# Optimization experiments

Measured on AMD Instinct MI355X. Metric: run time of the kernel, lower is better.

## Reference

```python
import jax, jax.numpy as jnp
import numpy as np

TAU = 10.0
AMP_FACTOR = 6.0
BLOCK = 10  # each pixel -> 8x8 value block padded by 1 -> 10x10


def _make_h(size=200, wavelength=5.32e-07, pixel_size=3.6e-05, distance=0.1):
    ll = pixel_size * size
    fi = 1.0 / ll
    wn = 2 * 3.1415926 / wavelength
    phi = np.fromfunction(
        lambda x, y: np.square((x - size // 2) * fi) + np.square((y - size // 2) * fi),
        shape=(size, size), dtype=np.float64)
    h = np.fft.fftshift(np.exp(1j * wn * distance) * np.exp(-1j * wavelength * np.pi * distance * phi))
    return h.astype(np.complex64)


def setup_inputs() -> dict:
    key = jax.random.key(0)
    B, S, P = 16, 200, 256
    ks = jax.random.split(key, 5)
    h = _make_h(size=S)
    return {
        "waves_real": jax.random.normal(ks[0], (B, S, S), jnp.float32),
        "waves_imag": jax.random.normal(ks[1], (B, S, S), jnp.float32),
        "h_real": jnp.asarray(h.real, jnp.float32),
        "h_imag": jnp.asarray(h.imag, jnp.float32),
        "voltage": jax.random.uniform(ks[2], (S, S, P), jnp.float32),
        "phase_func": jax.random.uniform(ks[3], (P,), jnp.float32),
        "intensity_func": jax.random.uniform(ks[4], (P,), jnp.float32),
    }


def _gumbel_softmax_hard(logits, key, tau):
    u = jax.random.uniform(key, logits.shape, logits.dtype, 1e-10, 1.0)
    g = -jnp.log(-jnp.log(u))
    y_soft = jax.nn.softmax((logits + g) / tau, axis=-1)
    y_hard = jax.nn.one_hot(jnp.argmax(y_soft, axis=-1), logits.shape[-1], dtype=logits.dtype)
    # straight-through estimator
    return y_hard + y_soft - jax.lax.stop_gradient(y_soft)


def reference(waves_real, waves_imag, h_real, h_imag, voltage, phase_func, intensity_func):
    waves = waves_real + 1j * waves_imag              # (B,S,S) complex
    h = h_real + 1j * h_imag                          # (S,S) complex transfer fn
    temp = jnp.fft.ifft2(jnp.fft.fft2(waves) * h)     # free-space diffraction

    k1, k2 = jax.random.split(jax.random.key(42))
    exp_j_phase = _gumbel_softmax_hard(voltage, k1, TAU) @ phase_func      # (S,S)
    amplitude = (_gumbel_softmax_hard(voltage, k2, TAU) @ intensity_func) * AMP_FACTOR
    phase_trig = amplitude * (jnp.cos(exp_j_phase) + 1j * jnp.sin(exp_j_phase))
    x = temp * phase_trig                             # (B,S,S) complex

    # pixel expansion: each pixel -> 10x10 block (value in center 8x8, zero border)
    B, S = x.shape[0], x.shape[1]
    pat = jnp.zeros((BLOCK, BLOCK), x.dtype).at[1:9, 1:9].set(1.0)
    out = (x[:, :, None, :, None] * pat[None, :, None, :][None]).reshape(B, S * BLOCK, S * BLOCK)
    return jnp.stack([out.real, out.imag], axis=-1)   # (B, 10S, 10S, 2) float
```

## Files before the change

kernel.cpp:

```cpp
#include <hip/hip_runtime.h>
#include <math.h>

constexpr int S = 200;
constexpr int SS = S * S;
constexpr int FLAT = 3200;
constexpr int SLICE = 640000;
constexpr int MP = 256;
constexpr int KP = 224;
constexpr int PS = MP * KP;

typedef short short8 __attribute__((ext_vector_type(8)));
typedef float float4v __attribute__((ext_vector_type(4)));

struct TFOut { unsigned a, b; };

__host__ __device__ constexpr TFOut tf2x32(unsigned k0, unsigned k1,
                                           unsigned x0, unsigned x1) {
  unsigned ks2 = k0 ^ k1 ^ 0x1BD11BDAu;
  unsigned ks[3] = {k0, k1, ks2};
  const int R0[4] = {13, 15, 26, 6};
  const int R1[4] = {17, 29, 16, 24};
  x0 += ks[0]; x1 += ks[1];
  for (int i = 0; i < 5; ++i) {
    const int* R = (i & 1) ? R1 : R0;
    for (int j = 0; j < 4; ++j) {
      x0 += x1;
      x1 = (x1 << R[j]) | (x1 >> (32 - R[j]));
      x1 ^= x0;
    }
    x0 += ks[(i + 1) % 3];
    x1 += ks[(i + 2) % 3] + (unsigned)(i + 1);
  }
  return {x0, x1};
}

constexpr TFOut KEY1 = tf2x32(0u, 42u, 0u, 0u);
constexpr TFOut KEY2 = tf2x32(0u, 42u, 0u, 1u);

__device__ inline float bits_to_u(unsigned bits) {
  float f = __uint_as_float((bits >> 9) | 0x3f800000u) - 1.0f;
  f = f + 1e-10f;
  return fmaxf(1e-10f, f);
}
__device__ inline float u_to_g_exact(float u) {
  float l1 = (float)log((double)u);
  float l2 = (float)log((double)(-l1));
  return -l2;
}
__device__ inline float u_to_g_fast(float u) {
  float l1 = logf(u);
  float l2 = logf(-l1);
  return -l2;
}
__device__ inline unsigned ordf(float f) {
  unsigned u = __float_as_uint(f);
  return (u & 0x80000000u) ? ~u : (u | 0x80000000u);
}
__device__ inline float unordf(unsigned u) {
  return (u & 0x80000000u) ? __uint_as_float(u ^ 0x80000000u)
                           : __uint_as_float(~u);
}
__device__ inline unsigned long long packcand(float val, int p) {
  return ((unsigned long long)ordf(val) << 32) | (unsigned)(255 - p);
}
__device__ inline unsigned long long umax64(unsigned long long a,
                                            unsigned long long b) {
  return a > b ? a : b;
}
__device__ inline unsigned long long wave_max_ull(unsigned long long v) {
#pragma unroll
  for (int s = 32; s > 0; s >>= 1)
    v = umax64(v, (unsigned long long)__shfl_xor((unsigned long long)v, s, 64));
  return v;
}

__global__ __launch_bounds__(256) void gumbel_kernel(
    const float* __restrict__ voltage, const float* __restrict__ phase_func,
    const float* __restrict__ intensity_func, float2* __restrict__ PT) {
  const int q = blockIdx.x;
  const int p = threadIdx.x;
  const int wave = p >> 6, lane = p & 63;
  const unsigned idx = (unsigned)q * 256u + (unsigned)p;
  const float v = voltage[(size_t)q * 256 + p];
  TFOut r1 = tf2x32(KEY1.a, KEY1.b, 0u, idx);
  TFOut r2 = tf2x32(KEY2.a, KEY2.b, 0u, idx);
  const float u1 = bits_to_u(r1.a ^ r1.b);
  const float u2 = bits_to_u(r2.a ^ r2.b);
  const float c1a = (v + u_to_g_fast(u1)) * 0.1f;
  const float c2a = (v + u_to_g_fast(u2)) * 0.1f;

  __shared__ unsigned long long wred[2][4];
  __shared__ int wcnt[2][4];

  unsigned long long pk1 = wave_max_ull(packcand(c1a, p));
  unsigned long long pk2 = wave_max_ull(packcand(c2a, p));
  if (lane == 0) { wred[0][wave] = pk1; wred[1][wave] = pk2; }
  __syncthreads();
  unsigned long long b1 = umax64(umax64(wred[0][0], wred[0][1]),
                                 umax64(wred[0][2], wred[0][3]));
  unsigned long long b2 = umax64(umax64(wred[1][0], wred[1][1]),
                                 umax64(wred[1][2], wred[1][3]));
  const float eps = 1e-5f;
  const bool q1 = c1a >= unordf((unsigned)(b1 >> 32)) - eps;
  const bool q2 = c2a >= unordf((unsigned)(b2 >> 32)) - eps;
  unsigned long long bal1 = __ballot(q1);
  unsigned long long bal2 = __ballot(q2);
  if (lane == 0) { wcnt[0][wave] = __popcll(bal1); wcnt[1][wave] = __popcll(bal2); }
  __syncthreads();
  const int n1 = wcnt[0][0] + wcnt[0][1] + wcnt[0][2] + wcnt[0][3];
  const int n2 = wcnt[1][0] + wcnt[1][1] + wcnt[1][2] + wcnt[1][3];

  unsigned long long w1 = b1, w2 = b2;
  if (n1 > 1 || n2 > 1) {
    unsigned long long e1 = q1 ? packcand((v + u_to_g_exact(u1)) / 10.0f, p) : 0ull;
    unsigned long long e2 = q2 ? packcand((v + u_to_g_exact(u2)) / 10.0f, p) : 0ull;
    e1 = wave_max_ull(e1);
    e2 = wave_max_ull(e2);
    if (lane == 0) { wred[0][wave] = e1; wred[1][wave] = e2; }
    __syncthreads();
    w1 = umax64(umax64(wred[0][0], wred[0][1]), umax64(wred[0][2], wred[0][3]));
    w2 = umax64(umax64(wred[1][0], wred[1][1]), umax64(wred[1][2], wred[1][3]));
  }
  if (p == 0) {
    int i1 = 255 - (int)(w1 & 0xFFFFFFFFull);
    int i2 = 255 - (int)(w2 & 0xFFFFFFFFull);
    float phi = phase_func[i1];
    float amp = intensity_func[i2] * 6.0f;
    PT[q] = make_float2(amp * cosf(phi), amp * sinf(phi));
  }
}

__global__ __launch_bounds__(256) void build_tw(float2* __restrict__ tw) {
  int m = threadIdx.x;
  if (m < S) {
    double ang = -2.0 * 3.1415926535897932384626433832795 * (double)m / (double)S;
    tw[m] = make_float2((float)cos(ang), (float)sin(ang));
  }
}

__device__ inline unsigned short bf16_rne(float x) {
  unsigned u = __float_as_uint(x);
  return (unsigned short)((u + 0x7FFFu + ((u >> 16) & 1u)) >> 16);
}
__device__ inline void split_bf16(float x, unsigned short& h, unsigned short& l) {
  h = bf16_rne(x);
  float hf = __uint_as_float(((unsigned)h) << 16);
  l = bf16_rne(x - hf);
}

__global__ __launch_bounds__(256) void build_planes(
    const float2* __restrict__ tw, unsigned short* __restrict__ PL) {
  int idx = blockIdx.x * 256 + threadIdx.x;
  int m = idx / KP, k = idx - (idx / KP) * KP;
  float fr = 0.f, fi = 0.f;
  if (m < S && k < S) {
    float2 t = tw[(m * k) % S];
    fr = t.x; fi = t.y;
  }
  unsigned short h, l;
  split_bf16(fr, h, l);          PL[0 * PS + idx] = h; PL[1 * PS + idx] = l;
  split_bf16(fi, h, l);          PL[2 * PS + idx] = h; PL[3 * PS + idx] = l;
  split_bf16(fr * 0.005f, h, l); PL[4 * PS + idx] = h; PL[5 * PS + idx] = l;
  split_bf16(-fi * 0.005f, h, l);PL[6 * PS + idx] = h; PL[7 * PS + idx] = l;
}

__global__ __launch_bounds__(256) void build_ht(
    const float* __restrict__ h_real, const float* __restrict__ h_imag,
    float2* __restrict__ HT) {
  int idx = blockIdx.x * 256 + threadIdx.x;
  if (idx >= SS) return;
  int k = idx / S, n = idx - (idx / S) * S;
  HT[n * S + k] = make_float2(h_real[idx], h_imag[idx]);
}

template <int MODE, bool FINAL>
__global__ __launch_bounds__(256) void gemm_mfma(
    const unsigned short* __restrict__ APL, const float* __restrict__ Wre,
    const float* __restrict__ Wim, const float2* __restrict__ Sprev,
    const float2* __restrict__ HT, const float2* __restrict__ PT,
    float2* __restrict__ Sout) {
  __shared__ short As[4][64][40];
  __shared__ short Bs[4][64][40];
  const int tid = threadIdx.x;
  const int wave = tid >> 6, lane = tid & 63, quad = lane >> 4, l15 = lane & 15;
  const int mb = blockIdx.x * 64;
  const int cb = blockIdx.y * 64;

  const int sp = tid >> 6;
  const int sm = tid & 63;
  const int sn = tid & 63;
  const int sk0 = (tid >> 6) * 8;
  const int cB = cb + sn;
  const int bB = cB / S;
  const int nB = cB - bB * S;

  float4v accRR[2][2], accII[2][2], accRI[2][2], accIR[2][2];
#pragma unroll
  for (int i = 0; i < 2; ++i)
#pragma unroll
    for (int j = 0; j < 2; ++j) {
      accRR[i][j] = (float4v){0.f, 0.f, 0.f, 0.f};
      accII[i][j] = (float4v){0.f, 0.f, 0.f, 0.f};
      accRI[i][j] = (float4v){0.f, 0.f, 0.f, 0.f};
      accIR[i][j] = (float4v){0.f, 0.f, 0.f, 0.f};
    }

  for (int ch = 0; ch < 7; ++ch) {
    const int kc = ch * 32;
    const unsigned short* ap = APL + sp * PS + (mb + sm) * KP + kc;
    short8 a0 = *(const short8*)(ap + 0);
    short8 a1 = *(const short8*)(ap + 8);
    short8 a2 = *(const short8*)(ap + 16);
    short8 a3 = *(const short8*)(ap + 24);

    unsigned short brh[8], brl[8], bih[8], bil[8];
    const bool kok = (kc + sk0) < S;
    float re[8], im[8];
#pragma unroll
    for (int j = 0; j < 8; ++j) { re[j] = 0.f; im[j] = 0.f; }
    if (kok) {
      if (MODE == 0) {
#pragma unroll
        for (int j = 0; j < 8; ++j) {
          int k = kc + sk0 + j;
          re[j] = Wre[(long)bB * SS + k * S + nB];
          im[j] = Wim[(long)bB * SS + k * S + nB];
        }
      } else {
        const float2* bp = &Sprev[(long)(bB * S + nB) * S + kc + sk0];
#pragma unroll
        for (int j = 0; j < 8; ++j) { re[j] = bp[j].x; im[j] = bp[j].y; }
        if (MODE == 2) {
          const float2* hp = &HT[(long)nB * S + kc + sk0];
#pragma unroll
          for (int j = 0; j < 8; ++j) {
            float2 hv = hp[j];
            float tr = re[j] * hv.x - im[j] * hv.y;
            im[j] = re[j] * hv.y + im[j] * hv.x;
            re[j] = tr;
          }
        }
      }
    }
#pragma unroll
    for (int j = 0; j < 8; ++j) {
      split_bf16(re[j], brh[j], brl[j]);
      split_bf16(im[j], bih[j], bil[j]);
    }

    __syncthreads();
    *(short8*)&As[sp][sm][0] = a0;
    *(short8*)&As[sp][sm][8] = a1;
    *(short8*)&As[sp][sm][16] = a2;
    *(short8*)&As[sp][sm][24] = a3;
    short8 v0, v1, v2, v3;
#pragma unroll
    for (int j = 0; j < 8; ++j) {
      v0[j] = (short)brh[j]; v1[j] = (short)brl[j];
      v2[j] = (short)bih[j]; v3[j] = (short)bil[j];
    }
    *(short8*)&Bs[0][sn][sk0] = v0;
    *(short8*)&Bs[1][sn][sk0] = v1;
    *(short8*)&Bs[2][sn][sk0] = v2;
    *(short8*)&Bs[3][sn][sk0] = v3;
    __syncthreads();

    short8 Arh[2], Arl[2], Aih[2], Ail[2], Brh[2], Brl[2], Bih[2], Bil[2];
#pragma unroll
    for (int t = 0; t < 2; ++t) {
      int mr = (wave & 1) * 32 + t * 16 + l15;
      Arh[t] = *(const short8*)&As[0][mr][quad * 8];
      Arl[t] = *(const short8*)&As[1][mr][quad * 8];
      Aih[t] = *(const short8*)&As[2][mr][quad * 8];
      Ail[t] = *(const short8*)&As[3][mr][quad * 8];
      int nr = (wave >> 1) * 32 + t * 16 + l15;
      Brh[t] = *(const short8*)&Bs[0][nr][quad * 8];
      Brl[t] = *(const short8*)&Bs[1][nr][quad * 8];
      Bih[t] = *(const short8*)&Bs[2][nr][quad * 8];
      Bil[t] = *(const short8*)&Bs[3][nr][quad * 8];
    }
#pragma unroll
    for (int mi = 0; mi < 2; ++mi)
#pragma unroll
      for (int ni = 0; ni < 2; ++ni) {
        accRR[mi][ni] = __builtin_amdgcn_mfma_f32_16x16x32_bf16(Arh[mi], Brh[ni], accRR[mi][ni], 0, 0, 0);
        accRR[mi][ni] = __builtin_amdgcn_mfma_f32_16x16x32_bf16(Arh[mi], Brl[ni], accRR[mi][ni], 0, 0, 0);
        accRR[mi][ni] = __builtin_amdgcn_mfma_f32_16x16x32_bf16(Arl[mi], Brh[ni], accRR[mi][ni], 0, 0, 0);
        accII[mi][ni] = __builtin_amdgcn_mfma_f32_16x16x32_bf16(Aih[mi], Bih[ni], accII[mi][ni], 0, 0, 0);
        accII[mi][ni] = __builtin_amdgcn_mfma_f32_16x16x32_bf16(Aih[mi], Bil[ni], accII[mi][ni], 0, 0, 0);
        accII[mi][ni] = __builtin_amdgcn_mfma_f32_16x16x32_bf16(Ail[mi], Bih[ni], accII[mi][ni], 0, 0, 0);
        accRI[mi][ni] = __builtin_amdgcn_mfma_f32_16x16x32_bf16(Arh[mi], Bih[ni], accRI[mi][ni], 0, 0, 0);
        accRI[mi][ni] = __builtin_amdgcn_mfma_f32_16x16x32_bf16(Arh[mi], Bil[ni], accRI[mi][ni], 0, 0, 0);
        accRI[mi][ni] = __builtin_amdgcn_mfma_f32_16x16x32_bf16(Arl[mi], Bih[ni], accRI[mi][ni], 0, 0, 0);
        accIR[mi][ni] = __builtin_amdgcn_mfma_f32_16x16x32_bf16(Aih[mi], Brh[ni], accIR[mi][ni], 0, 0, 0);
        accIR[mi][ni] = __builtin_amdgcn_mfma_f32_16x16x32_bf16(Aih[mi], Brl[ni], accIR[mi][ni], 0, 0, 0);
        accIR[mi][ni] = __builtin_amdgcn_mfma_f32_16x16x32_bf16(Ail[mi], Brh[ni], accIR[mi][ni], 0, 0, 0);
      }
  }

#pragma unroll
  for (int mi = 0; mi < 2; ++mi)
#pragma unroll
    for (int ni = 0; ni < 2; ++ni) {
      int cg = cb + (wave >> 1) * 32 + ni * 16 + l15;
      int b = cg / S;
      int n = cg - b * S;
#pragma unroll
      for (int r = 0; r < 4; ++r) {
        int m = mb + (wave & 1) * 32 + mi * 16 + quad * 4 + r;
        if (m < S) {
          float Cr = accRR[mi][ni][r] - accII[mi][ni][r];
          float Ci = accRI[mi][ni][r] + accIR[mi][ni][r];
          if (FINAL) {
            float2 pt = PT[n * S + m];
            float tr = Cr * pt.x - Ci * pt.y;
            Ci = Cr * pt.y + Ci * pt.x;
            Cr = tr;
          }
          Sout[(long)(b * S + m) * S + n] = make_float2(Cr, Ci);
        }
      }
    }
}

__global__ __launch_bounds__(256) void expand_kernel(
    const float2* __restrict__ S4, float4* __restrict__ out) {
  unsigned q = blockIdx.x * 256u + threadIdx.x;
  unsigned p0 = q * 2u;
  unsigned b = p0 / 4000000u;
  unsigned rem = p0 - b * 4000000u;
  unsigned r = rem / 2000u;
  unsigned c0 = rem - r * 2000u;
  unsigned i = r / 10u;
  unsigned dr = r - i * 10u;
  float4 o = {0.f, 0.f, 0.f, 0.f};
  if (dr - 1u <= 7u) {
    unsigned j = c0 / 10u;
    unsigned dc = c0 - j * 10u;
    float2 xv = S4[(b * 200u + j) * 200u + i];
    if (dc != 0u) { o.x = xv.x; o.y = xv.y; }
    if (dc != 8u) { o.z = xv.x; o.w = xv.y; }
  }
  out[q] = o;
}

extern "C" void kernel_launch(void* const* d_in, const int* in_sizes, int n_in,
                              void* d_out, int out_size, void* d_ws, size_t ws_size,
                              hipStream_t stream) {
  const float* waves_real = (const float*)d_in[0];
  const float* waves_imag = (const float*)d_in[1];
  const float* h_real = (const float*)d_in[2];
  const float* h_imag = (const float*)d_in[3];
  const float* voltage = (const float*)d_in[4];
  const float* phase_func = (const float*)d_in[5];
  const float* intensity_func = (const float*)d_in[6];

  float2* TW = (float2*)d_ws;
  float2* HT = TW + 256;
  float2* PT = HT + SS;
  float2* S1 = PT + SS;
  float2* S2 = S1 + SLICE;
  float2* S3 = S2 + SLICE;
  float2* S4 = S3 + SLICE;
  unsigned short* PL = (unsigned short*)(S4 + SLICE);

  build_tw<<<1, 256, 0, stream>>>(TW);
  build_planes<<<224, 256, 0, stream>>>(TW, PL);
  build_ht<<<157, 256, 0, stream>>>(h_real, h_imag, HT);
  gumbel_kernel<<<40000, 256, 0, stream>>>(voltage, phase_func, intensity_func, PT);

  const unsigned short* FP = PL;
  const unsigned short* GP = PL + 4 * PS;
  dim3 g(4, 50);
  gemm_mfma<0, false><<<g, 256, 0, stream>>>(FP, waves_real, waves_imag,
                                             nullptr, nullptr, nullptr, S1);
  gemm_mfma<1, false><<<g, 256, 0, stream>>>(FP, nullptr, nullptr, S1,
                                             nullptr, nullptr, S2);
  gemm_mfma<2, false><<<g, 256, 0, stream>>>(GP, nullptr, nullptr, S2,
                                             HT, nullptr, S3);
  gemm_mfma<1, true><<<g, 256, 0, stream>>>(GP, nullptr, nullptr, S3,
                                            nullptr, PT, S4);

  expand_kernel<<<125000, 256, 0, stream>>>(S4, (float4*)d_out);
}
```

Before: 681.8 us.

## Shrink GEMM tiles to 32x32, fuse HT build, use nontemporal output stores

Reduces the MFMA GEMM block tile from 64x64 to 32x32 and pads M to 224 instead of 256, so the grid grows from 200 to 700 blocks, which gives the GPU more blocks to run in parallel and wastes fewer padded rows. It also merges the transposed-H build into the DFT plane builder to save a launch. The output expansion kernel writes with nontemporal stores to avoid polluting cache on the large write-only output. Smaller tiles lower data reuse per block and add more loads per MFMA.

```diff
diff --git a/kernel.cpp b/kernel.cpp
--- a/kernel.cpp
+++ b/kernel.cpp
@@ -3,13 +3,13 @@
 
 constexpr int S = 200;
 constexpr int SS = S * S;
-constexpr int FLAT = 3200;
 constexpr int SLICE = 640000;
-constexpr int MP = 256;
+constexpr int MP = 224;
 constexpr int KP = 224;
 constexpr int PS = MP * KP;
 
 typedef short short8 __attribute__((ext_vector_type(8)));
+typedef short short4v __attribute__((ext_vector_type(4)));
 typedef float float4v __attribute__((ext_vector_type(4)));
 
 struct TFOut { unsigned a, b; };
@@ -148,8 +148,10 @@
   l = bf16_rne(x - hf);
 }
 
-__global__ __launch_bounds__(256) void build_planes(
-    const float2* __restrict__ tw, unsigned short* __restrict__ PL) {
+__global__ __launch_bounds__(256) void build_planes_ht(
+    const float2* __restrict__ tw, const float* __restrict__ h_real,
+    const float* __restrict__ h_imag, unsigned short* __restrict__ PL,
+    float2* __restrict__ HT) {
   int idx = blockIdx.x * 256 + threadIdx.x;
   int m = idx / KP, k = idx - (idx / KP) * KP;
   float fr = 0.f, fi = 0.f;
@@ -158,19 +160,14 @@
     fr = t.x; fi = t.y;
   }
   unsigned short h, l;
-  split_bf16(fr, h, l);          PL[0 * PS + idx] = h; PL[1 * PS + idx] = l;
-  split_bf16(fi, h, l);          PL[2 * PS + idx] = h; PL[3 * PS + idx] = l;
-  split_bf16(fr * 0.005f, h, l); PL[4 * PS + idx] = h; PL[5 * PS + idx] = l;
-  split_bf16(-fi * 0.005f, h, l);PL[6 * PS + idx] = h; PL[7 * PS + idx] = l;
-}
-
-__global__ __launch_bounds__(256) void build_ht(
-    const float* __restrict__ h_real, const float* __restrict__ h_imag,
-    float2* __restrict__ HT) {
-  int idx = blockIdx.x * 256 + threadIdx.x;
-  if (idx >= SS) return;
-  int k = idx / S, n = idx - (idx / S) * S;
-  HT[n * S + k] = make_float2(h_real[idx], h_imag[idx]);
+  split_bf16(fr, h, l);           PL[0 * PS + idx] = h; PL[1 * PS + idx] = l;
+  split_bf16(fi, h, l);           PL[2 * PS + idx] = h; PL[3 * PS + idx] = l;
+  split_bf16(fr * 0.005f, h, l);  PL[4 * PS + idx] = h; PL[5 * PS + idx] = l;
+  split_bf16(-fi * 0.005f, h, l); PL[6 * PS + idx] = h; PL[7 * PS + idx] = l;
+  if (idx < SS) {
+    int kk = idx / S, n = idx - (idx / S) * S;
+    HT[n * S + kk] = make_float2(h_real[idx], h_imag[idx]);
+  }
 }
 
 template <int MODE, bool FINAL>
@@ -179,61 +176,52 @@
     const float* __restrict__ Wim, const float2* __restrict__ Sprev,
     const float2* __restrict__ HT, const float2* __restrict__ PT,
     float2* __restrict__ Sout) {
-  __shared__ short As[4][64][40];
-  __shared__ short Bs[4][64][40];
+  __shared__ short As[4][32][40];
+  __shared__ short Bs[4][32][40];
   const int tid = threadIdx.x;
   const int wave = tid >> 6, lane = tid & 63, quad = lane >> 4, l15 = lane & 15;
-  const int mb = blockIdx.x * 64;
-  const int cb = blockIdx.y * 64;
-
-  const int sp = tid >> 6;
-  const int sm = tid & 63;
-  const int sn = tid & 63;
-  const int sk0 = (tid >> 6) * 8;
-  const int cB = cb + sn;
+  const int mb = blockIdx.x * 32;
+  const int cb = blockIdx.y * 32;
+  const int mh = wave & 1, nh = wave >> 1;
+
+  const int ap_ = tid >> 6;
+  const int ar = (tid & 63) >> 1;
+  const int ag = (tid & 1) * 8;
+  const unsigned short* abase = APL + ap_ * PS + (mb + ar) * KP;
+
+  const int bc = tid >> 3;
+  const int bkq = (tid & 7) * 4;
+  const int cB = cb + bc;
   const int bB = cB / S;
   const int nB = cB - bB * S;
 
-  float4v accRR[2][2], accII[2][2], accRI[2][2], accIR[2][2];
-#pragma unroll
-  for (int i = 0; i < 2; ++i)
-#pragma unroll
-    for (int j = 0; j < 2; ++j) {
-      accRR[i][j] = (float4v){0.f, 0.f, 0.f, 0.f};
-      accII[i][j] = (float4v){0.f, 0.f, 0.f, 0.f};
-      accRI[i][j] = (float4v){0.f, 0.f, 0.f, 0.f};
-      accIR[i][j] = (float4v){0.f, 0.f, 0.f, 0.f};
-    }
+  float4v accRR = {0.f, 0.f, 0.f, 0.f}, accII = {0.f, 0.f, 0.f, 0.f};
+  float4v accRI = {0.f, 0.f, 0.f, 0.f}, accIR = {0.f, 0.f, 0.f, 0.f};
 
   for (int ch = 0; ch < 7; ++ch) {
     const int kc = ch * 32;
-    const unsigned short* ap = APL + sp * PS + (mb + sm) * KP + kc;
-    short8 a0 = *(const short8*)(ap + 0);
-    short8 a1 = *(const short8*)(ap + 8);
-    short8 a2 = *(const short8*)(ap + 16);
-    short8 a3 = *(const short8*)(ap + 24);
-
-    unsigned short brh[8], brl[8], bih[8], bil[8];
-    const bool kok = (kc + sk0) < S;
-    float re[8], im[8];
-#pragma unroll
-    for (int j = 0; j < 8; ++j) { re[j] = 0.f; im[j] = 0.f; }
-    if (kok) {
+    short8 a0 = *(const short8*)(abase + kc + ag);
+    short8 a1 = *(const short8*)(abase + kc + ag + 16);
+
+    float re[4], im[4];
+#pragma unroll
+    for (int j = 0; j < 4; ++j) { re[j] = 0.f; im[j] = 0.f; }
+    const int gk = kc + bkq;
+    if (gk < S) {
       if (MODE == 0) {
 #pragma unroll
-        for (int j = 0; j < 8; ++j) {
-          int k = kc + sk0 + j;
-          re[j] = Wre[(long)bB * SS + k * S + nB];
-          im[j] = Wim[(long)bB * SS + k * S + nB];
+        for (int j = 0; j < 4; ++j) {
+          re[j] = Wre[(long)bB * SS + (gk + j) * S + nB];
+          im[j] = Wim[(long)bB * SS + (gk + j) * S + nB];
         }
       } else {
-        const float2* bp = &Sprev[(long)(bB * S + nB) * S + kc + sk0];
-#pragma unroll
-        for (int j = 0; j < 8; ++j) { re[j] = bp[j].x; im[j] = bp[j].y; }
+        const float2* bp = &Sprev[(long)(bB * S + nB) * S + gk];
+#pragma unroll
+        for (int j = 0; j < 4; ++j) { re[j] = bp[j].x; im[j] = bp[j].y; }
         if (MODE == 2) {
-          const float2* hp = &HT[(long)nB * S + kc + sk0];
-#pragma unroll
-          for (int j = 0; j < 8; ++j) {
+          const float2* hp = &HT[(long)nB * S + gk];
+#pragma unroll
+          for (int j = 0; j < 4; ++j) {
             float2 hv = hp[j];
             float tr = re[j] * hv.x - im[j] * hv.y;
             im[j] = re[j] * hv.y + im[j] * hv.x;
@@ -242,89 +230,70 @@
         }
       }
     }
-#pragma unroll
-    for (int j = 0; j < 8; ++j) {
-      split_bf16(re[j], brh[j], brl[j]);
-      split_bf16(im[j], bih[j], bil[j]);
+    short4v rh, rl, ih, il;
+#pragma unroll
+    for (int j = 0; j < 4; ++j) {
+      unsigned short h_, l_;
+      split_bf16(re[j], h_, l_); rh[j] = (short)h_; rl[j] = (short)l_;
+      split_bf16(im[j], h_, l_); ih[j] = (short)h_; il[j] = (short)l_;
     }
 
     __syncthreads();
-    *(short8*)&As[sp][sm][0] = a0;
-    *(short8*)&As[sp][sm][8] = a1;
-    *(short8*)&As[sp][sm][16] = a2;
-    *(short8*)&As[sp][sm][24] = a3;
-    short8 v0, v1, v2, v3;
-#pragma unroll
-    for (int j = 0; j < 8; ++j) {
-      v0[j] = (short)brh[j]; v1[j] = (short)brl[j];
-      v2[j] = (short)bih[j]; v3[j] = (short)bil[j];
+    *(short8*)&As[ap_][ar][ag] = a0;
+    *(short8*)&As[ap_][ar][ag + 16] = a1;
+    *(short4v*)&Bs[0][bc][bkq] = rh;
+    *(short4v*)&Bs[1][bc][bkq] = rl;
+    *(short4v*)&Bs[2][bc][bkq] = ih;
+    *(short4v*)&Bs[3][bc][bkq] = il;
+    __syncthreads();
+
+    const int amr = mh * 16 + l15;
+    const int bnr = nh * 16 + l15;
+    short8 Arh = *(const short8*)&As[0][amr][quad * 8];
+    short8 Arl = *(const short8*)&As[1][amr][quad * 8];
+    short8 Aih = *(const short8*)&As[2][amr][quad * 8];
+    short8 Ail = *(const short8*)&As[3][amr][quad * 8];
+    short8 Brh = *(const short8*)&Bs[0][bnr][quad * 8];
+    short8 Brl = *(const short8*)&Bs[1][bnr][quad * 8];
+    short8 Bih = *(const short8*)&Bs[2][bnr][quad * 8];
+    short8 Bil = *(const short8*)&Bs[3][bnr][quad * 8];
+
+    accRR = __builtin_amdgcn_mfma_f32_16x16x32_bf16(Arh, Brh, accRR, 0, 0, 0);
+    accRR = __builtin_amdgcn_mfma_f32_16x16x32_bf16(Arh, Brl, accRR, 0, 0, 0);
+    accRR = __builtin_amdgcn_mfma_f32_16x16x32_bf16(Arl, Brh, accRR, 0, 0, 0);
+    accII = __builtin_amdgcn_mfma_f32_16x16x32_bf16(Aih, Bih, accII, 0, 0, 0);
+    accII = __builtin_amdgcn_mfma_f32_16x16x32_bf16(Aih, Bil, accII, 0, 0, 0);
+    accII = __builtin_amdgcn_mfma_f32_16x16x32_bf16(Ail, Bih, accII, 0, 0, 0);
+    accRI = __builtin_amdgcn_mfma_f32_16x16x32_bf16(Arh, Bih, accRI, 0, 0, 0);
+    accRI = __builtin_amdgcn_mfma_f32_16x16x32_bf16(Arh, Bil, accRI, 0, 0, 0);
+    accRI = __builtin_amdgcn_mfma_f32_16x16x32_bf16(Arl, Bih, accRI, 0, 0, 0);
+    accIR = __builtin_amdgcn_mfma_f32_16x16x32_bf16(Aih, Brh, accIR, 0, 0, 0);
+    accIR = __builtin_amdgcn_mfma_f32_16x16x32_bf16(Aih, Brl, accIR, 0, 0, 0);
+    accIR = __builtin_amdgcn_mfma_f32_16x16x32_bf16(Ail, Brh, accIR, 0, 0, 0);
+  }
+
+  const int cg = cb + nh * 16 + l15;
+  const int b = cg / S;
+  const int n = cg - b * S;
+#pragma unroll
+  for (int r = 0; r < 4; ++r) {
+    const int m = mb + mh * 16 + quad * 4 + r;
+    if (m < S) {
+      float Cr = accRR[r] - accII[r];
+      float Ci = accRI[r] + accIR[r];
+      if (FINAL) {
+        float2 pt = PT[n * S + m];
+        float tr = Cr * pt.x - Ci * pt.y;
+        Ci = Cr * pt.y + Ci * pt.x;
+        Cr = tr;
+      }
+      Sout[(long)(b * S + m) * S + n] = make_float2(Cr, Ci);
     }
-    *(short8*)&Bs[0][sn][sk0] = v0;
-    *(short8*)&Bs[1][sn][sk0] = v1;
-    *(short8*)&Bs[2][sn][sk0] = v2;
-    *(short8*)&Bs[3][sn][sk0] = v3;
-    __syncthreads();
-
-    short8 Arh[2], Arl[2], Aih[2], Ail[2], Brh[2], Brl[2], Bih[2], Bil[2];
-#pragma unroll
-    for (int t = 0; t < 2; ++t) {
-      int mr = (wave & 1) * 32 + t * 16 + l15;
-      Arh[t] = *(const short8*)&As[0][mr][quad * 8];
-      Arl[t] = *(const short8*)&As[1][mr][quad * 8];
-      Aih[t] = *(const short8*)&As[2][mr][quad * 8];
-      Ail[t] = *(const short8*)&As[3][mr][quad * 8];
-      int nr = (wave >> 1) * 32 + t * 16 + l15;
-      Brh[t] = *(const short8*)&Bs[0][nr][quad * 8];
-      Brl[t] = *(const short8*)&Bs[1][nr][quad * 8];
-      Bih[t] = *(const short8*)&Bs[2][nr][quad * 8];
-      Bil[t] = *(const short8*)&Bs[3][nr][quad * 8];
-    }
-#pragma unroll
-    for (int mi = 0; mi < 2; ++mi)
-#pragma unroll
-      for (int ni = 0; ni < 2; ++ni) {
-        accRR[mi][ni] = __builtin_amdgcn_mfma_f32_16x16x32_bf16(Arh[mi], Brh[ni], accRR[mi][ni], 0, 0, 0);
-        accRR[mi][ni] = __builtin_amdgcn_mfma_f32_16x16x32_bf16(Arh[mi], Brl[ni], accRR[mi][ni], 0, 0, 0);
-        accRR[mi][ni] = __builtin_amdgcn_mfma_f32_16x16x32_bf16(Arl[mi], Brh[ni], accRR[mi][ni], 0, 0, 0);
-        accII[mi][ni] = __builtin_amdgcn_mfma_f32_16x16x32_bf16(Aih[mi], Bih[ni], accII[mi][ni], 0, 0, 0);
-        accII[mi][ni] = __builtin_amdgcn_mfma_f32_16x16x32_bf16(Aih[mi], Bil[ni], accII[mi][ni], 0, 0, 0);
-        accII[mi][ni] = __builtin_amdgcn_mfma_f32_16x16x32_bf16(Ail[mi], Bih[ni], accII[mi][ni], 0, 0, 0);
-        accRI[mi][ni] = __builtin_amdgcn_mfma_f32_16x16x32_bf16(Arh[mi], Bih[ni], accRI[mi][ni], 0, 0, 0);
-        accRI[mi][ni] = __builtin_amdgcn_mfma_f32_16x16x32_bf16(Arh[mi], Bil[ni], accRI[mi][ni], 0, 0, 0);
-        accRI[mi][ni] = __builtin_amdgcn_mfma_f32_16x16x32_bf16(Arl[mi], Bih[ni], accRI[mi][ni], 0, 0, 0);
-        accIR[mi][ni] = __builtin_amdgcn_mfma_f32_16x16x32_bf16(Aih[mi], Brh[ni], accIR[mi][ni], 0, 0, 0);
-        accIR[mi][ni] = __builtin_amdgcn_mfma_f32_16x16x32_bf16(Aih[mi], Brl[ni], accIR[mi][ni], 0, 0, 0);
-        accIR[mi][ni] = __builtin_amdgcn_mfma_f32_16x16x32_bf16(Ail[mi], Brh[ni], accIR[mi][ni], 0, 0, 0);
-      }
-  }
-
-#pragma unroll
-  for (int mi = 0; mi < 2; ++mi)
-#pragma unroll
-    for (int ni = 0; ni < 2; ++ni) {
-      int cg = cb + (wave >> 1) * 32 + ni * 16 + l15;
-      int b = cg / S;
-      int n = cg - b * S;
-#pragma unroll
-      for (int r = 0; r < 4; ++r) {
-        int m = mb + (wave & 1) * 32 + mi * 16 + quad * 4 + r;
-        if (m < S) {
-          float Cr = accRR[mi][ni][r] - accII[mi][ni][r];
-          float Ci = accRI[mi][ni][r] + accIR[mi][ni][r];
-          if (FINAL) {
-            float2 pt = PT[n * S + m];
-            float tr = Cr * pt.x - Ci * pt.y;
-            Ci = Cr * pt.y + Ci * pt.x;
-            Cr = tr;
-          }
-          Sout[(long)(b * S + m) * S + n] = make_float2(Cr, Ci);
-        }
-      }
-    }
+  }
 }
 
 __global__ __launch_bounds__(256) void expand_kernel(
-    const float2* __restrict__ S4, float4* __restrict__ out) {
+    const float2* __restrict__ S4, float4v* __restrict__ out) {
   unsigned q = blockIdx.x * 256u + threadIdx.x;
   unsigned p0 = q * 2u;
   unsigned b = p0 / 4000000u;
@@ -333,7 +302,7 @@
   unsigned c0 = rem - r * 2000u;
   unsigned i = r / 10u;
   unsigned dr = r - i * 10u;
-  float4 o = {0.f, 0.f, 0.f, 0.f};
+  float4v o = {0.f, 0.f, 0.f, 0.f};
   if (dr - 1u <= 7u) {
     unsigned j = c0 / 10u;
     unsigned dc = c0 - j * 10u;
@@ -341,7 +310,7 @@
     if (dc != 0u) { o.x = xv.x; o.y = xv.y; }
     if (dc != 8u) { o.z = xv.x; o.w = xv.y; }
   }
-  out[q] = o;
+  __builtin_nontemporal_store(o, &out[q]);
 }
 
 extern "C" void kernel_launch(void* const* d_in, const int* in_sizes, int n_in,
@@ -365,13 +334,12 @@
   unsigned short* PL = (unsigned short*)(S4 + SLICE);
 
   build_tw<<<1, 256, 0, stream>>>(TW);
-  build_planes<<<224, 256, 0, stream>>>(TW, PL);
-  build_ht<<<157, 256, 0, stream>>>(h_real, h_imag, HT);
+  build_planes_ht<<<196, 256, 0, stream>>>(TW, h_real, h_imag, PL, HT);
   gumbel_kernel<<<40000, 256, 0, stream>>>(voltage, phase_func, intensity_func, PT);
 
   const unsigned short* FP = PL;
   const unsigned short* GP = PL + 4 * PS;
-  dim3 g(4, 50);
+  dim3 g(7, 100);
   gemm_mfma<0, false><<<g, 256, 0, stream>>>(FP, waves_real, waves_imag,
                                              nullptr, nullptr, nullptr, S1);
   gemm_mfma<1, false><<<g, 256, 0, stream>>>(FP, nullptr, nullptr, S1,
@@ -381,5 +349,5 @@
   gemm_mfma<1, true><<<g, 256, 0, stream>>>(GP, nullptr, nullptr, S3,
                                             nullptr, PT, S4);
 
-  expand_kernel<<<125000, 256, 0, stream>>>(S4, (float4*)d_out);
-}
+  expand_kernel<<<125000, 256, 0, stream>>>(S4, (float4v*)d_out);
+}
```

New measurement: 635.3 us. 6.8% less time.
